# Kernel tuning notes

Measured on AMD Instinct MI355X. Metric: run time of the kernel, lower is better.

The kernel has to match this reference:

```python
import jax, jax.numpy as jnp
import numpy as np
import math

V, D, H, F, L = 32000, 1024, 16, 4096, 6
B, S_DEC, S_ENC = 8, 512, 512
EPS = 1e-5


def _pos_encoding(seq_len, d_model):
    pos = jnp.arange(seq_len, dtype=jnp.float32)[:, None]
    div = jnp.exp(jnp.arange(0, d_model, 2, dtype=jnp.float32) * (-math.log(10000.0) / d_model))
    pe = jnp.zeros((seq_len, d_model), dtype=jnp.float32)
    pe = pe.at[:, 0::2].set(jnp.sin(pos * div))
    pe = pe.at[:, 1::2].set(jnp.cos(pos * div))
    return pe


def _layernorm(x, g, b):
    m = jnp.mean(x, axis=-1, keepdims=True)
    v = jnp.mean((x - m) ** 2, axis=-1, keepdims=True)
    return (x - m) * jax.lax.rsqrt(v + EPS) * g + b


def _mha(q_in, k_in, v_in, w, b, mask, n_heads):
    # w: [4, D, D] stored as [in, out] (q,k,v,o); b: [4, D]
    bsz, sq, dm = q_in.shape
    hd = dm // n_heads
    q = (q_in @ w[0] + b[0]).reshape(bsz, sq, n_heads, hd)
    k = (k_in @ w[1] + b[1]).reshape(bsz, -1, n_heads, hd)
    v = (v_in @ w[2] + b[2]).reshape(bsz, -1, n_heads, hd)
    scores = jnp.einsum('bqhd,bkhd->bhqk', q, k) / jnp.sqrt(jnp.asarray(hd, q.dtype))
    if mask is not None:
        scores = jnp.where(mask, jnp.asarray(-1e15, scores.dtype), scores)
    att = jax.nn.softmax(scores, axis=-1)
    out = jnp.einsum('bhqk,bkhd->bqhd', att, v).reshape(bsz, sq, dm)
    return out @ w[3] + b[3]


def setup_inputs() -> dict:
    key = jax.random.key(0)
    ks = jax.random.split(key, 16)
    sc = 0.02
    enc_out = jax.random.normal(ks[0], (B, S_ENC, D), dtype=jnp.float32)
    dec_in = jax.random.randint(ks[1], (B, S_DEC), 0, V, dtype=jnp.int64)
    # no padding on encoder side
    enc_dec_mask = jnp.zeros((1, 1, S_DEC, S_ENC), dtype=bool)
    # causal mask: True above the diagonal -> masked out
    fut_mask = jnp.triu(jnp.ones((S_DEC, S_DEC), dtype=bool), k=1)[None, None]
    return {
        'encoder_output': enc_out,
        'decoder_input': dec_in,
        'encoder_decoder_mask': enc_dec_mask,
        'decoder_future_mask': fut_mask,
        'embed_table': jax.random.normal(ks[2], (V, D), dtype=jnp.float32) * sc,
        'sa_w': jax.random.normal(ks[3], (L, 4, D, D), dtype=jnp.float32) * sc,
        'sa_b': jnp.zeros((L, 4, D), dtype=jnp.float32),
        'ca_w': jax.random.normal(ks[4], (L, 4, D, D), dtype=jnp.float32) * sc,
        'ca_b': jnp.zeros((L, 4, D), dtype=jnp.float32),
        'ffn_w1': jax.random.normal(ks[5], (L, D, F), dtype=jnp.float32) * sc,
        'ffn_b1': jnp.zeros((L, F), dtype=jnp.float32),
        'ffn_w2': jax.random.normal(ks[6], (L, F, D), dtype=jnp.float32) * sc,
        'ffn_b2': jnp.zeros((L, D), dtype=jnp.float32),
        'ln_g': jnp.ones((L, 3, D), dtype=jnp.float32),
        'ln_b': jnp.zeros((L, 3, D), dtype=jnp.float32),
        'final_g': jnp.ones((D,), dtype=jnp.float32),
        'final_b': jnp.zeros((D,), dtype=jnp.float32),
    }


def reference(encoder_output, decoder_input, encoder_decoder_mask, decoder_future_mask,
              embed_table, sa_w, sa_b, ca_w, ca_b, ffn_w1, ffn_b1, ffn_w2, ffn_b2,
              ln_g, ln_b, final_g, final_b):
    seq_len = decoder_input.shape[1]
    x = embed_table[decoder_input] * jnp.asarray(math.sqrt(D), jnp.float32)
    x = x + _pos_encoding(seq_len, D)
    for l in range(L):
        # pre-norm self-attention (dropout is identity at eval)
        h = _layernorm(x, ln_g[l, 0], ln_b[l, 0])
        x = x + _mha(h, h, h, sa_w[l], sa_b[l], decoder_future_mask, H)
        # pre-norm cross-attention
        h = _layernorm(x, ln_g[l, 1], ln_b[l, 1])
        x = x + _mha(h, encoder_output, encoder_output, ca_w[l], ca_b[l], encoder_decoder_mask, H)
        # pre-norm FFN
        h = _layernorm(x, ln_g[l, 2], ln_b[l, 2])
        x = x + jax.nn.relu(h @ ffn_w1[l] + ffn_b1[l]) @ ffn_w2[l] + ffn_b2[l]
    return _layernorm(x, final_g, final_b)
```

## Files before the change

kernel.cpp:

```cpp
#include <hip/hip_runtime.h>
#include <hip/hip_bf16.h>

typedef __attribute__((ext_vector_type(8))) short bf16x8;
typedef __attribute__((ext_vector_type(4))) float f32x4;
typedef __hip_bfloat16 bf16;

constexpr int DM   = 1024;
constexpr int NH   = 16;
constexpr int HD   = 64;
constexpr int FF   = 4096;
constexpr int NL   = 6;
constexpr int NB_  = 8;
constexpr int SEQL = 512;
constexpr int NTOK = NB_ * SEQL;

__device__ __forceinline__ void gl_lds16(const void* g, void* l) {
  __builtin_amdgcn_global_load_lds(
      (const __attribute__((address_space(1))) unsigned int*)g,
      (__attribute__((address_space(3))) unsigned int*)l, 16, 0, 0);
}

__global__ __launch_bounds__(256) void transpose_cvt(const float* __restrict__ src,
                                                     bf16* __restrict__ dst,
                                                     int R, int C) {
  __shared__ float tile[32][33];
  size_t mo = (size_t)blockIdx.z * R * C;
  src += mo; dst += mo;
  int c0 = blockIdx.x * 32, r0 = blockIdx.y * 32;
  int tx = threadIdx.x, ty = threadIdx.y;
  #pragma unroll
  for (int j = 0; j < 4; ++j)
    tile[ty + 8*j][tx] = src[(size_t)(r0 + ty + 8*j) * C + c0 + tx];
  __syncthreads();
  #pragma unroll
  for (int j = 0; j < 4; ++j)
    dst[(size_t)(c0 + ty + 8*j) * R + r0 + tx] = __float2bfloat16(tile[tx][ty + 8*j]);
}

__global__ __launch_bounds__(256) void cvt_bf16(const float* __restrict__ s,
                                                bf16* __restrict__ d) {
  size_t i = (size_t)blockIdx.x * 256 + threadIdx.x;
  float4 v = ((const float4*)s)[i];
  union { bf16 h[4]; uint2 u; } t;
  t.h[0] = __float2bfloat16(v.x); t.h[1] = __float2bfloat16(v.y);
  t.h[2] = __float2bfloat16(v.z); t.h[3] = __float2bfloat16(v.w);
  *(uint2*)(d + i * 4) = t.u;
}

__global__ __launch_bounds__(256) void vtrans(const bf16* __restrict__ in,
                                              bf16* __restrict__ out) {
  __shared__ bf16 tile[32][33];
  int t0 = blockIdx.x * 32, d0 = blockIdx.y * 32;
  int tx = threadIdx.x, ty = threadIdx.y;
  #pragma unroll
  for (int j = 0; j < 4; ++j)
    tile[ty + 8*j][tx] = in[(size_t)(t0 + ty + 8*j) * 3072 + 2048 + d0 + tx];
  __syncthreads();
  #pragma unroll
  for (int j = 0; j < 4; ++j)
    out[(size_t)(d0 + ty + 8*j) * NTOK + t0 + tx] = tile[tx][ty + 8*j];
}

__global__ __launch_bounds__(256) void embed_pe(const int* __restrict__ tok,
                                                const float* __restrict__ table,
                                                float* __restrict__ x) {
  int t = blockIdx.x;
  int s = t & (SEQL - 1);
  int tk = tok[t];
  int d = threadIdx.x * 4;
  float4 e = *(const float4*)(table + (size_t)tk * DM + d);
  float o[4] = {e.x, e.y, e.z, e.w};
  const float NEGC = -9.210340371976184f / 1024.0f;
  #pragma unroll
  for (int i = 0; i < 4; ++i) {
    int dd = d + i;
    float div = __expf((float)(dd & ~1) * NEGC);
    float arg = (float)s * div;
    float pe = (dd & 1) ? cosf(arg) : sinf(arg);
    o[i] = o[i] * 32.0f + pe;
  }
  float4 ov = {o[0], o[1], o[2], o[3]};
  *(float4*)(x + (size_t)t * DM + d) = ov;
}

__device__ __forceinline__ void ln_wave(float4 v[4], const float* __restrict__ g,
                                        const float* __restrict__ bb,
                                        int row, int lane, bf16* ob, float* of, int outf32) {
  float s = 0.0f;
  #pragma unroll
  for (int i = 0; i < 4; ++i) s += v[i].x + v[i].y + v[i].z + v[i].w;
  #pragma unroll
  for (int o = 32; o; o >>= 1) s += __shfl_xor(s, o);
  float mean = s * (1.0f / DM);
  float s2 = 0.0f;
  #pragma unroll
  for (int i = 0; i < 4; ++i) {
    v[i].x -= mean; v[i].y -= mean; v[i].z -= mean; v[i].w -= mean;
    s2 += v[i].x*v[i].x + v[i].y*v[i].y + v[i].z*v[i].z + v[i].w*v[i].w;
  }
  #pragma unroll
  for (int o = 32; o; o >>= 1) s2 += __shfl_xor(s2, o);
  float rs = rsqrtf(s2 * (1.0f / DM) + 1e-5f);
  #pragma unroll
  for (int i = 0; i < 4; ++i) {
    int c = (lane + i * 64) * 4;
    float4 gg = *(const float4*)(g + c);
    float4 bv = *(const float4*)(bb + c);
    float y0 = v[i].x * rs * gg.x + bv.x;
    float y1 = v[i].y * rs * gg.y + bv.y;
    float y2 = v[i].z * rs * gg.z + bv.z;
    float y3 = v[i].w * rs * gg.w + bv.w;
    if (outf32) {
      float4 ov = {y0, y1, y2, y3};
      *(float4*)(of + (size_t)row * DM + c) = ov;
    } else {
      union { bf16 h[4]; uint2 u; } t;
      t.h[0] = __float2bfloat16(y0); t.h[1] = __float2bfloat16(y1);
      t.h[2] = __float2bfloat16(y2); t.h[3] = __float2bfloat16(y3);
      *(uint2*)(ob + (size_t)row * DM + c) = t.u;
    }
  }
}

template<int OUTF32>
__global__ __launch_bounds__(256) void ln_kernel(const float* __restrict__ x,
                                                 const float* __restrict__ g,
                                                 const float* __restrict__ bb,
                                                 bf16* __restrict__ ob,
                                                 float* __restrict__ of) {
  int wv = threadIdx.x >> 6, lane = threadIdx.x & 63;
  int row = blockIdx.x * 4 + wv;
  const float4* xr = (const float4*)(x + (size_t)row * DM);
  float4 v[4];
  #pragma unroll
  for (int i = 0; i < 4; ++i) v[i] = xr[lane + i * 64];
  ln_wave(v, g, bb, row, lane, ob, of, OUTF32);
}

template<int OUTF32>
__global__ __launch_bounds__(256) void ln_fused(float* __restrict__ x,
                                                const float* __restrict__ p,
                                                const float* __restrict__ bias,
                                                const float* __restrict__ g,
                                                const float* __restrict__ bb,
                                                bf16* __restrict__ ob,
                                                float* __restrict__ of) {
  int wv = threadIdx.x >> 6, lane = threadIdx.x & 63;
  int row = blockIdx.x * 4 + wv;
  size_t rb = (size_t)row * DM;
  const size_t NM = (size_t)NTOK * DM;
  float4 v[4];
  #pragma unroll
  for (int i = 0; i < 4; ++i) {
    int c = (lane + i * 64) * 4;
    float4 xv = *(const float4*)(x + rb + c);
    float4 a0 = *(const float4*)(p + rb + c);
    float4 a1 = *(const float4*)(p + NM + rb + c);
    float4 bv = *(const float4*)(bias + c);
    xv.x += a0.x + a1.x + bv.x;
    xv.y += a0.y + a1.y + bv.y;
    xv.z += a0.z + a1.z + bv.z;
    xv.w += a0.w + a1.w + bv.w;
    *(float4*)(x + rb + c) = xv;
    v[i] = xv;
  }
  ln_wave(v, g, bb, row, lane, ob, of, OUTF32);
}

template<int EPI, int BN>
__global__ __launch_bounds__(256) void gemm_bt(const bf16* __restrict__ A,
                                               const bf16* __restrict__ Bt,
                                               const float* __restrict__ bias,
                                               bf16* __restrict__ Cb,
                                               float* __restrict__ Cf,
                                               int M, int N, int K) {
  constexpr int NFR = BN / 32;
  constexpr int BCH = BN / 64;
  __shared__ bf16 As[3][128 * 32];
  __shared__ bf16 Bs[3][BN * 32];
  int tid = threadIdx.x;
  int wave = tid >> 6, lane = tid & 63;
  int l4 = lane & 15, lhi = lane >> 4;
  int wr = wave >> 1, wc = wave & 1;
  int nwg = gridDim.x * gridDim.y;
  int bid = blockIdx.y * gridDim.x + blockIdx.x;
  int cpx = nwg >> 3;
  int swz = (bid & 7) * cpx + (bid >> 3);
  int bx = swz % gridDim.x, by = swz / gridDim.x;
  int brow = by * 128, bcol = bx * BN;
  f32x4 acc[4][NFR] = {};
  int srow = lane >> 2;
  int scol = (lane & 3) * 8;

  int kbase = 0, Keff = K;
  if (EPI == 4) { Keff = K >> 1; kbase = blockIdx.z * Keff; }
  int T = Keff >> 5;

  auto stage = [&](int buf, int t) {
    int k0 = kbase + t * 32;
    #pragma unroll
    for (int i = 0; i < 2; ++i) {
      int rr = brow + i * 64 + wave * 16;
      if (EPI == 6) rr = ((rr >> 10) << 12) + 2048 + (rr & 1023);
      gl_lds16(A + (size_t)(rr + srow) * K + k0 + scol, &As[buf][(i * 64 + wave * 16) * 32]);
    }
    #pragma unroll
    for (int i = 0; i < BCH; ++i) {
      int rr = bcol + i * 64 + wave * 16;
      if (EPI == 5) rr = ((rr >> 10) << 12) + 1024 + (rr & 1023);
      gl_lds16(Bt + (size_t)(rr + srow) * K + k0 + scol, &Bs[buf][(i * 64 + wave * 16) * 32]);
    }
  };
  auto compute = [&](int buf) {
    bf16x8 af[4], bfv[NFR];
    #pragma unroll
    for (int m = 0; m < 4; ++m)
      af[m] = *(const bf16x8*)&As[buf][(wr * 64 + m * 16 + l4) * 32 + lhi * 8];
    #pragma unroll
    for (int n = 0; n < NFR; ++n)
      bfv[n] = *(const bf16x8*)&Bs[buf][(wc * (BN / 2) + n * 16 + l4) * 32 + lhi * 8];
    #pragma unroll
    for (int m = 0; m < 4; ++m)
      #pragma unroll
      for (int n = 0; n < NFR; ++n)
        acc[m][n] = __builtin_amdgcn_mfma_f32_16x16x32_bf16(af[m], bfv[n], acc[m][n], 0, 0, 0);
  };

  stage(0, 0);
  stage(1, 1);
  for (int t = 0; t < T; ++t) {
    if (t < T - 1) {
      if constexpr (BN == 128) asm volatile("s_waitcnt vmcnt(4)" ::: "memory");
      else                     asm volatile("s_waitcnt vmcnt(3)" ::: "memory");
    } else {
      asm volatile("s_waitcnt vmcnt(0)" ::: "memory");
    }
    __builtin_amdgcn_s_barrier();
    asm volatile("" ::: "memory");
    if (t + 2 < T) stage((t + 2) % 3, t + 2);
    compute(t % 3);
  }

  #pragma unroll
  for (int m = 0; m < 4; ++m) {
    int row0 = brow + wr * 64 + m * 16 + lhi * 4;
    #pragma unroll
    for (int n = 0; n < NFR; ++n) {
      int col = bcol + wc * (BN / 2) + n * 16 + l4;
      #pragma unroll
      for (int r = 0; r < 4; ++r) {
        int row = row0 + r;
        float v = acc[m][n][r];
        if (EPI == 0) {
          v += bias[col];
          Cb[(size_t)row * N + col] = __float2bfloat16(v);
        } else if (EPI == 1) {
          v += bias[col];
          v = fmaxf(v, 0.0f);
          Cb[(size_t)row * N + col] = __float2bfloat16(v);
        } else if (EPI == 3) {
          v += bias[col];
          size_t idx = (size_t)row * N + col;
          Cf[idx] = Cf[idx] + v;
        } else if (EPI == 4) {
          Cf[(size_t)blockIdx.z * ((size_t)M * N) + (size_t)row * N + col] = v;
        } else if (EPI == 5) {
          v += bias[((col >> 10) << 12) + 1024 + (col & 1023)];
          Cb[(size_t)row * N + col] = __float2bfloat16(v);
        } else {
          v += bias[((row >> 10) << 12) + 2048 + (row & 1023)];
          Cb[(size_t)row * N + col] = __float2bfloat16(v);
        }
      }
    }
  }
}

template<int CAUSAL>
__global__ __launch_bounds__(256, 2) void attn_kernel(const bf16* __restrict__ qg,
                                                      const bf16* __restrict__ kg,
                                                      const bf16* __restrict__ vtg,
                                                      bf16* __restrict__ og,
                                                      int qs, int ks) {
  __shared__ bf16 P[4][16][520];
  __shared__ bf16 KV[4096];
  int qblk = blockIdx.x;
  int bh = blockIdx.y;
  int b = bh >> 4, h = bh & 15;
  int wave = threadIdx.x >> 6, lane = threadIdx.x & 63;
  int l4 = lane & 15, lhi = lane >> 4;
  int qbase = qblk * 64 + wave * 16;
  const int qmax = CAUSAL ? (qbase + 15) : 0x7fffffff;
  const int tmaxb = CAUSAL ? qblk : 7;

  int srow8 = lane >> 3;
  int sbyte = ((lane & 7) * 16) ^ (srow8 << 4);
  int rdswz = (l4 & 7) << 4;

  bf16x8 qa[2];
  {
    size_t qrow = (size_t)(b * SEQL + qbase + l4);
    #pragma unroll
    for (int kk = 0; kk < 2; ++kk)
      qa[kk] = *(const bf16x8*)&qg[qrow * qs + h * HD + kk * 32 + lhi * 8];
  }

  f32x4 acc[32] = {};
  #pragma unroll
  for (int t = 0; t < 8; ++t) {
    if (t <= tmaxb) {
      #pragma unroll
      for (int j = 0; j < 2; ++j) {
        int row = (wave * 2 + j) * 8 + srow8;
        const char* src = (const char*)(kg + (size_t)(b * SEQL + t * 64 + row) * ks + h * HD) + sbyte;
        gl_lds16(src, (char*)&KV[0] + (wave * 2 + j) * 1024);
      }
      asm volatile("s_waitcnt vmcnt(0)" ::: "memory");
      __builtin_amdgcn_s_barrier();
      asm volatile("" ::: "memory");
      #pragma unroll
      for (int n = 0; n < 4; ++n) {
        int nk = t * 4 + n;
        if (!CAUSAL || nk * 16 <= qmax) {
          #pragma unroll
          for (int kk = 0; kk < 2; ++kk) {
            bf16x8 kf = *(const bf16x8*)((const char*)&KV[0] + (n * 16 + l4) * 128 + ((kk * 64 + lhi * 16) ^ rdswz));
            acc[nk] = __builtin_amdgcn_mfma_f32_16x16x32_bf16(qa[kk], kf, acc[nk], 0, 0, 0);
          }
        }
      }
      __builtin_amdgcn_s_barrier();
      asm volatile("" ::: "memory");
    }
  }

  int qloc = qbase + lhi * 4;
  #pragma unroll
  for (int r = 0; r < 4; ++r) {
    float mx = -3.0e38f;
    #pragma unroll
    for (int n = 0; n < 32; ++n) {
      float sv = acc[n][r] * 0.125f;
      if (CAUSAL && (n * 16 + l4 > qloc + r)) sv = -3.0e38f;
      acc[n][r] = sv;
      mx = fmaxf(mx, sv);
    }
    #pragma unroll
    for (int o = 1; o < 16; o <<= 1) mx = fmaxf(mx, __shfl_xor(mx, o));
    float sum = 0.0f;
    #pragma unroll
    for (int n = 0; n < 32; ++n) {
      float p;
      if (CAUSAL && n * 16 > qmax) p = 0.0f;
      else p = __expf(acc[n][r] - mx);
      acc[n][r] = p;
      sum += p;
    }
    #pragma unroll
    for (int o = 1; o < 16; o <<= 1) sum += __shfl_xor(sum, o);
    float rcp = 1.0f / sum;
    #pragma unroll
    for (int n = 0; n < 32; ++n)
      P[wave][lhi * 4 + r][n * 16 + l4] = __float2bfloat16(acc[n][r] * rcp);
  }

  f32x4 oacc[4] = {};
  #pragma unroll
  for (int t = 0; t < 8; ++t) {
    if (t <= tmaxb) {
      #pragma unroll
      for (int j = 0; j < 2; ++j) {
        int row = (wave * 2 + j) * 8 + srow8;
        const char* src = (const char*)(vtg + (size_t)(h * HD + row) * NTOK + b * SEQL + t * 64) + sbyte;
        gl_lds16(src, (char*)&KV[0] + (wave * 2 + j) * 1024);
      }
      asm volatile("s_waitcnt vmcnt(0)" ::: "memory");
      __builtin_amdgcn_s_barrier();
      asm volatile("" ::: "memory");
      #pragma unroll
      for (int ksl = 0; ksl < 2; ++ksl) {
        int kslot = t * 2 + ksl;
        if (!CAUSAL || kslot * 32 <= qmax) {
          bf16x8 pa = *(const bf16x8*)&P[wave][l4][kslot * 32 + lhi * 8];
          #pragma unroll
          for (int nn = 0; nn < 4; ++nn) {
            bf16x8 vf = *(const bf16x8*)((const char*)&KV[0] + (nn * 16 + l4) * 128 + ((ksl * 64 + lhi * 16) ^ rdswz));
            oacc[nn] = __builtin_amdgcn_mfma_f32_16x16x32_bf16(pa, vf, oacc[nn], 0, 0, 0);
          }
        }
      }
      __builtin_amdgcn_s_barrier();
      asm volatile("" ::: "memory");
    }
  }

  size_t orow = (size_t)(b * SEQL + qbase + lhi * 4);
  #pragma unroll
  for (int n = 0; n < 4; ++n)
    #pragma unroll
    for (int r = 0; r < 4; ++r)
      og[(orow + r) * DM + h * HD + n * 16 + l4] = __float2bfloat16(oacc[n][r]);
}

extern "C" void kernel_launch(void* const* d_in, const int* in_sizes, int n_in,
                              void* d_out, int out_size, void* d_ws, size_t ws_size,
                              hipStream_t stream) {
  (void)in_sizes; (void)n_in; (void)out_size;
  const float* enc   = (const float*)d_in[0];
  const int*   toks  = (const int*)  d_in[1];
  const float* table = (const float*)d_in[4];
  const float* sa_w  = (const float*)d_in[5];
  const float* sa_b  = (const float*)d_in[6];
  const float* ca_w  = (const float*)d_in[7];
  const float* ca_b  = (const float*)d_in[8];
  const float* f1w   = (const float*)d_in[9];
  const float* f1b   = (const float*)d_in[10];
  const float* f2w   = (const float*)d_in[11];
  const float* f2b   = (const float*)d_in[12];
  const float* lng   = (const float*)d_in[13];
  const float* lnbp  = (const float*)d_in[14];
  const float* fg    = (const float*)d_in[15];
  const float* fbp   = (const float*)d_in[16];
  float* outp = (float*)d_out;

  char* base = (char*)d_ws;
  size_t off = 0;
  auto alloc = [&](size_t nbytes) -> char* {
    char* p = base + off;
    off += (nbytes + 255) & ~(size_t)255;
    return p;
  };
  const size_t DDb = (size_t)DM * DM;
  bf16* wt_sa   = (bf16*)alloc((size_t)NL * 4 * DDb * 2);
  bf16* wt_ca   = (bf16*)alloc((size_t)NL * 4 * DDb * 2);
  bf16* wt_f1   = (bf16*)alloc((size_t)NL * FF * DM * 2);
  bf16* wt_f2   = (bf16*)alloc((size_t)NL * FF * DM * 2);
  bf16* encb    = (bf16*)alloc((size_t)NTOK * DM * 2);
  bf16* keall   = (bf16*)alloc((size_t)NTOK * NL * DM * 2);
  bf16* vteall  = (bf16*)alloc((size_t)NL * DM * NTOK * 2);
  bf16* hbuf    = (bf16*)alloc((size_t)NTOK * DM * 2);
  bf16* qkvbuf  = (bf16*)alloc((size_t)NTOK * 3 * DM * 2);
  bf16* vtbuf   = (bf16*)alloc((size_t)NTOK * DM * 2);
  bf16* aobuf   = (bf16*)alloc((size_t)NTOK * DM * 2);
  bf16* h1buf   = (bf16*)alloc((size_t)NTOK * FF * 2);
  float* xbuf   = (float*)alloc((size_t)NTOK * DM * 4);
  float* pbuf   = (float*)alloc((size_t)2 * NTOK * DM * 4);
  if (off > ws_size) return;

  dim3 tb(32, 8);
  transpose_cvt<<<dim3(DM/32, DM/32, NL*4), tb, 0, stream>>>(sa_w, wt_sa, DM, DM);
  transpose_cvt<<<dim3(DM/32, DM/32, NL*4), tb, 0, stream>>>(ca_w, wt_ca, DM, DM);
  transpose_cvt<<<dim3(FF/32, DM/32, NL),   tb, 0, stream>>>(f1w, wt_f1, DM, FF);
  transpose_cvt<<<dim3(DM/32, FF/32, NL),   tb, 0, stream>>>(f2w, wt_f2, FF, DM);
  cvt_bf16<<<(NTOK * DM / 4) / 256, 256, 0, stream>>>(enc, encb);
  embed_pe<<<NTOK, 256, 0, stream>>>(toks, table, xbuf);

  gemm_bt<5,128><<<dim3(NL*DM/128, NTOK/128), 256, 0, stream>>>(encb, wt_ca, ca_b, keall, nullptr, NTOK, NL*DM, DM);
  gemm_bt<6,128><<<dim3(NTOK/128, NL*DM/128), 256, 0, stream>>>(wt_ca, encb, ca_b, vteall, nullptr, NL*DM, NTOK, DM);

  ln_kernel<0><<<NTOK/4, 256, 0, stream>>>(xbuf, lng + 0*DM, lnbp + 0*DM, hbuf, nullptr);

  for (int l = 0; l < NL; ++l) {
    const bf16* wsa = wt_sa + (size_t)l * 4 * DDb;
    const bf16* wca = wt_ca + (size_t)l * 4 * DDb;
    const float* bsa = sa_b + (size_t)l * 4 * DM;
    const float* bca = ca_b + (size_t)l * 4 * DM;
    gemm_bt<0,128><<<dim3(3*DM/128, NTOK/128), 256, 0, stream>>>(hbuf, wsa, bsa, qkvbuf, nullptr, NTOK, 3*DM, DM);
    vtrans<<<dim3(NTOK/32, DM/32), tb, 0, stream>>>(qkvbuf, vtbuf);
    attn_kernel<1><<<dim3(SEQL/64, NB_*NH), 256, 0, stream>>>(qkvbuf, qkvbuf + DM, vtbuf, aobuf, 3*DM, 3*DM);
    gemm_bt<3,64><<<dim3(DM/64, NTOK/128), 256, 0, stream>>>(aobuf, wsa + 3*DDb, bsa + 3*DM, nullptr, xbuf, NTOK, DM, DM);
    ln_kernel<0><<<NTOK/4, 256, 0, stream>>>(xbuf, lng + (l*3+1)*DM, lnbp + (l*3+1)*DM, hbuf, nullptr);
    gemm_bt<0,64><<<dim3(DM/64, NTOK/128), 256, 0, stream>>>(hbuf, wca + 0*DDb, bca + 0*DM, qkvbuf, nullptr, NTOK, DM, DM);
    attn_kernel<0><<<dim3(SEQL/64, NB_*NH), 256, 0, stream>>>(qkvbuf, keall + l*DM, vteall + (size_t)l*DM*NTOK, aobuf, DM, NL*DM);
    gemm_bt<3,64><<<dim3(DM/64, NTOK/128), 256, 0, stream>>>(aobuf, wca + 3*DDb, bca + 3*DM, nullptr, xbuf, NTOK, DM, DM);
    ln_kernel<0><<<NTOK/4, 256, 0, stream>>>(xbuf, lng + (l*3+2)*DM, lnbp + (l*3+2)*DM, hbuf, nullptr);
    gemm_bt<1,128><<<dim3(FF/128, NTOK/128), 256, 0, stream>>>(hbuf, wt_f1 + (size_t)l*FF*DM, f1b + (size_t)l*FF, h1buf, nullptr, NTOK, FF, DM);
    gemm_bt<4,64><<<dim3(DM/64, NTOK/128, 2), 256, 0, stream>>>(h1buf, wt_f2 + (size_t)l*FF*DM, nullptr, nullptr, pbuf, NTOK, DM, FF);
    if (l < NL - 1)
      ln_fused<0><<<NTOK/4, 256, 0, stream>>>(xbuf, pbuf, f2b + (size_t)l*DM,
                                              lng + ((l+1)*3+0)*DM, lnbp + ((l+1)*3+0)*DM, hbuf, nullptr);
    else
      ln_fused<1><<<NTOK/4, 256, 0, stream>>>(xbuf, pbuf, f2b + (size_t)l*DM,
                                              fg, fbp, nullptr, outp);
  }
}
```

Before: 2.295 ms.

## Double-buffer K/V tiles in attention and swizzle workgroup order

Attention now stages K and V in 32-row tiles through two LDS buffers. The next tile's global-to-LDS load is issued before computing on the current one, so load latency overlaps MFMA work. Workgroup indices are also remapped so consecutive blocks come from different head/batch groups and query blocks, which spreads causal work more evenly and may change L2 locality. Halving the tile size doubles the number of barriers, and a new V swizzle layout is introduced.

```diff
diff --git a/kernel.cpp b/kernel.cpp
--- a/kernel.cpp
+++ b/kernel.cpp
@@ -283,19 +283,32 @@
                                                       bf16* __restrict__ og,
                                                       int qs, int ks) {
   __shared__ bf16 P[4][16][520];
-  __shared__ bf16 KV[4096];
-  int qblk = blockIdx.x;
-  int bh = blockIdx.y;
+  __shared__ bf16 KV2[2][2048];
+  int nwg = gridDim.x * gridDim.y;
+  int lin = blockIdx.y * gridDim.x + blockIdx.x;
+  int swzb = (lin & 7) * (nwg >> 3) + (lin >> 3);
+  int qblk = swzb & 7;
+  int bh = swzb >> 3;
   int b = bh >> 4, h = bh & 15;
   int wave = threadIdx.x >> 6, lane = threadIdx.x & 63;
   int l4 = lane & 15, lhi = lane >> 4;
   int qbase = qblk * 64 + wave * 16;
   const int qmax = CAUSAL ? (qbase + 15) : 0x7fffffff;
-  const int tmaxb = CAUSAL ? qblk : 7;
-
-  int srow8 = lane >> 3;
-  int sbyte = ((lane & 7) * 16) ^ (srow8 << 4);
-  int rdswz = (l4 & 7) << 4;
+  const int tmaxb = CAUSAL ? (2 * qblk + 1) : 15;
+
+  auto stageK = [&](int buf, int t) {
+    int row = wave * 8 + (lane >> 3);
+    const char* src = (const char*)(kg + (size_t)(b * SEQL + t * 32 + row) * ks + h * HD)
+                      + ((((lane & 7) * 16)) ^ ((lane >> 3) << 4));
+    gl_lds16(src, (char*)&KV2[buf][0] + wave * 1024);
+  };
+  auto stageV = [&](int buf, int t) {
+    int row = threadIdx.x >> 2;
+    int slot = (lane & 3) ^ ((row >> 1) & 3);
+    const char* src = (const char*)(vtg + (size_t)(h * HD + row) * NTOK + b * SEQL + t * 32)
+                      + slot * 16;
+    gl_lds16(src, (char*)&KV2[buf][0] + wave * 1024);
+  };
 
   bf16x8 qa[2];
   {
@@ -306,25 +319,27 @@
   }
 
   f32x4 acc[32] = {};
-  #pragma unroll
-  for (int t = 0; t < 8; ++t) {
+  int rdK = (l4 & 7) << 4;
+  stageK(0, 0);
+  #pragma unroll
+  for (int t = 0; t < 16; ++t) {
     if (t <= tmaxb) {
-      #pragma unroll
-      for (int j = 0; j < 2; ++j) {
-        int row = (wave * 2 + j) * 8 + srow8;
-        const char* src = (const char*)(kg + (size_t)(b * SEQL + t * 64 + row) * ks + h * HD) + sbyte;
-        gl_lds16(src, (char*)&KV[0] + (wave * 2 + j) * 1024);
+      if (t + 1 <= tmaxb) {
+        stageK((t + 1) & 1, t + 1);
+        asm volatile("s_waitcnt vmcnt(1)" ::: "memory");
+      } else {
+        asm volatile("s_waitcnt vmcnt(0)" ::: "memory");
       }
-      asm volatile("s_waitcnt vmcnt(0)" ::: "memory");
       __builtin_amdgcn_s_barrier();
       asm volatile("" ::: "memory");
+      const char* kb = (const char*)&KV2[t & 1][0];
       #pragma unroll
-      for (int n = 0; n < 4; ++n) {
-        int nk = t * 4 + n;
-        if (!CAUSAL || nk * 16 <= qmax) {
+      for (int g = 0; g < 2; ++g) {
+        int nk = t * 2 + g;
+        if (!CAUSAL || (t * 32 + g * 16) <= qmax) {
           #pragma unroll
           for (int kk = 0; kk < 2; ++kk) {
-            bf16x8 kf = *(const bf16x8*)((const char*)&KV[0] + (n * 16 + l4) * 128 + ((kk * 64 + lhi * 16) ^ rdswz));
+            bf16x8 kf = *(const bf16x8*)(kb + (g * 16 + l4) * 128 + ((kk * 64 + lhi * 16) ^ rdK));
             acc[nk] = __builtin_amdgcn_mfma_f32_16x16x32_bf16(qa[kk], kf, acc[nk], 0, 0, 0);
           }
         }
@@ -363,30 +378,29 @@
     for (int n = 0; n < 32; ++n)
       P[wave][lhi * 4 + r][n * 16 + l4] = __float2bfloat16(acc[n][r] * rcp);
   }
+  stageV(0, 0);
+  __syncthreads();
 
   f32x4 oacc[4] = {};
-  #pragma unroll
-  for (int t = 0; t < 8; ++t) {
+  int rdV = ((l4 >> 1) & 3) << 4;
+  #pragma unroll
+  for (int t = 0; t < 16; ++t) {
     if (t <= tmaxb) {
-      #pragma unroll
-      for (int j = 0; j < 2; ++j) {
-        int row = (wave * 2 + j) * 8 + srow8;
-        const char* src = (const char*)(vtg + (size_t)(h * HD + row) * NTOK + b * SEQL + t * 64) + sbyte;
-        gl_lds16(src, (char*)&KV[0] + (wave * 2 + j) * 1024);
+      if (t + 1 <= tmaxb) {
+        stageV((t + 1) & 1, t + 1);
+        asm volatile("s_waitcnt vmcnt(1)" ::: "memory");
+      } else {
+        asm volatile("s_waitcnt vmcnt(0)" ::: "memory");
       }
-      asm volatile("s_waitcnt vmcnt(0)" ::: "memory");
       __builtin_amdgcn_s_barrier();
       asm volatile("" ::: "memory");
-      #pragma unroll
-      for (int ksl = 0; ksl < 2; ++ksl) {
-        int kslot = t * 2 + ksl;
-        if (!CAUSAL || kslot * 32 <= qmax) {
-          bf16x8 pa = *(const bf16x8*)&P[wave][l4][kslot * 32 + lhi * 8];
-          #pragma unroll
-          for (int nn = 0; nn < 4; ++nn) {
-            bf16x8 vf = *(const bf16x8*)((const char*)&KV[0] + (nn * 16 + l4) * 128 + ((ksl * 64 + lhi * 16) ^ rdswz));
-            oacc[nn] = __builtin_amdgcn_mfma_f32_16x16x32_bf16(pa, vf, oacc[nn], 0, 0, 0);
-          }
+      if (!CAUSAL || t * 32 <= qmax) {
+        bf16x8 pa = *(const bf16x8*)&P[wave][l4][t * 32 + lhi * 8];
+        const char* vb = (const char*)&KV2[t & 1][0];
+        #pragma unroll
+        for (int nn = 0; nn < 4; ++nn) {
+          bf16x8 vf = *(const bf16x8*)(vb + (nn * 16 + l4) * 64 + ((lhi * 16) ^ rdV));
+          oacc[nn] = __builtin_amdgcn_mfma_f32_16x16x32_bf16(pa, vf, oacc[nn], 0, 0, 0);
         }
       }
       __builtin_amdgcn_s_barrier();
```

New measurement: 2.331 ms. Within noise of the previous version (+1.6%).
